# Kernel optimization log

Measured on AMD Instinct MI355X. Metric: run time of the kernel, lower is better.

## Reference

```python
import jax, jax.numpy as jnp
import numpy as np

T, B, S, H, E, V = 100, 64, 602, 1024, 512, 10000


def setup_inputs() -> dict:
    key = jax.random.key(0)
    ks = jax.random.split(key, 12)
    s = 0.02  # small init scale for numerical stability through tanh/sigmoid
    return {
        "tgt": jax.random.randint(ks[0], (T, B, 1), 0, V),
        "memory_bank": jax.random.normal(ks[1], (S, B, H), jnp.float32),
        "h0": jax.random.normal(ks[2], (2, B, H), jnp.float32) * 0.1,
        "c0": jax.random.normal(ks[3], (2, B, H), jnp.float32) * 0.1,
        "embedding": jax.random.normal(ks[4], (V, E), jnp.float32) * s,
        "Wi0": jax.random.normal(ks[5], (4 * H, E + H), jnp.float32) * s,
        "Wh0": jax.random.normal(ks[6], (4 * H, H), jnp.float32) * s,
        "bi0": jnp.zeros((4 * H,), jnp.float32),
        "bh0": jnp.zeros((4 * H,), jnp.float32),
        "Wi1": jax.random.normal(ks[7], (4 * H, H), jnp.float32) * s,
        "Wh1": jax.random.normal(ks[8], (4 * H, H), jnp.float32) * s,
        "bi1": jnp.zeros((4 * H,), jnp.float32),
        "bh1": jnp.zeros((4 * H,), jnp.float32),
        "W_attn": jax.random.normal(ks[9], (H, H), jnp.float32) * s,
        "W_out": jax.random.normal(ks[10], (H, 2 * H), jnp.float32) * s,
    }


def _lstm_cell(x, h, c, Wi, Wh, bi, bh):
    # PyTorch LSTM gate order: i, f, g, o
    g = x @ Wi.T + h @ Wh.T + bi + bh
    i, f, gg, o = jnp.split(g, 4, axis=-1)
    c2 = jax.nn.sigmoid(f) * c + jax.nn.sigmoid(i) * jnp.tanh(gg)
    h2 = jax.nn.sigmoid(o) * jnp.tanh(c2)
    return h2, c2


def reference(tgt, memory_bank, h0, c0, embedding, Wi0, Wh0, bi0, bh0,
              Wi1, Wh1, bi1, bh1, W_attn, W_out):
    emb = embedding[tgt[:, :, 0]]            # [T, B, E]
    M = jnp.transpose(memory_bank, (1, 0, 2))  # [B, S, H]

    def step(carry, e_t):
        hl0, hl1, cl0, cl1, feed = carry
        x = jnp.concatenate([e_t, feed], axis=-1)        # input feeding
        nh0, nc0 = _lstm_cell(x, hl0, cl0, Wi0, Wh0, bi0, bh0)
        nh1, nc1 = _lstm_cell(nh0, hl1, cl1, Wi1, Wh1, bi1, bh1)
        # GlobalAttention 'general': score = (h W) . m
        q = nh1 @ W_attn.T                                # [B, H]
        align = jnp.einsum('bh,bsh->bs', q, M)            # [B, S]
        a = jax.nn.softmax(align, axis=-1)
        ctx = jnp.einsum('bs,bsh->bh', a, M)              # [B, H]
        out = jnp.tanh(jnp.concatenate([ctx, nh1], -1) @ W_out.T)  # attn_h
        return (nh0, nh1, nc0, nc1, out), (out, a)

    init = (h0[0], h0[1], c0[0], c0[1], jnp.zeros((B, H), emb.dtype))
    (_, _, _, _, _), (outs, attns) = jax.lax.scan(step, init, emb)
    return outs, attns  # [T,B,H], [T,B,S]
```

## Files before the change

kernel.cpp:

```cpp
#include <hip/hip_runtime.h>


#define DI __device__ __forceinline__

typedef __attribute__((ext_vector_type(4))) short s4v;
typedef __attribute__((ext_vector_type(8))) short s8v;
typedef __attribute__((ext_vector_type(4))) float f4v;

DI float b2f(short u) {
  unsigned int x = ((unsigned int)(unsigned short)u) << 16;
  float f; __builtin_memcpy(&f, &x, 4); return f;
}
DI short f2b(float f) {
  unsigned int x; __builtin_memcpy(&x, &f, 4);
  return (short)((x + 0x7fffu + ((x >> 16) & 1u)) >> 16);
}
DI s8v cat8(s4v lo, s4v hi) {
  s8v r; r[0]=lo[0];r[1]=lo[1];r[2]=lo[2];r[3]=lo[3];
  r[4]=hi[0];r[5]=hi[1];r[6]=hi[2];r[7]=hi[3]; return r;
}
DI f4v mfma16(s8v a, s8v b, f4v c) {
  return __builtin_amdgcn_mfma_f32_16x16x32_bf16(a, b, c, 0, 0, 0);
}
DI float sigm(float x) { return 1.f / (1.f + __expf(-x)); }

DI unsigned long long ld64c(const void* p) {
  return __hip_atomic_load((const unsigned long long*)p, __ATOMIC_RELAXED,
                           __HIP_MEMORY_SCOPE_SYSTEM);
}
DI void st64c(void* p, unsigned long long v) {
  __hip_atomic_store((unsigned long long*)p, v, __ATOMIC_RELAXED,
                     __HIP_MEMORY_SCOPE_SYSTEM);
}
DI float ldfc(const float* p) {
  return __hip_atomic_load(p, __ATOMIC_RELAXED, __HIP_MEMORY_SCOPE_SYSTEM);
}
DI void stfc(float* p, float v) {
  __hip_atomic_store(p, v, __ATOMIC_RELAXED, __HIP_MEMORY_SCOPE_SYSTEM);
}
DI int ld32c(const int* p) {
  return __hip_atomic_load(p, __ATOMIC_RELAXED, __HIP_MEMORY_SCOPE_SYSTEM);
}
DI void st32c(int* p, int v) {
  __hip_atomic_store(p, v, __ATOMIC_RELAXED, __HIP_MEMORY_SCOPE_SYSTEM);
}
DI void st16c(short* p, short v) {
  asm volatile("global_store_short %0, %1, off sc0 sc1"
               :: "v"(p), "v"((unsigned int)(unsigned short)v) : "memory");
}
DI void st128c(void* p, s8v v) {
  asm volatile("global_store_dwordx4 %0, %1, off sc0 sc1"
               :: "v"(p), "v"(v) : "memory");
}
DI void st128cf(void* p, f4v v) {
  asm volatile("global_store_dwordx4 %0, %1, off sc0 sc1"
               :: "v"(p), "v"(v) : "memory");
}
union U64S { unsigned long long u; short s[4]; };
union U64F { unsigned long long u; float f[2]; };


__global__ void cvt_bf16(const float* __restrict__ src, short* __restrict__ dst, long n8) {
  long i = (long)blockIdx.x * blockDim.x + threadIdx.x;
  long stride = (long)gridDim.x * blockDim.x;
  for (; i < n8; i += stride) {
    const float* s = src + i * 8;
    s8v o;
    #pragma unroll
    for (int j = 0; j < 8; ++j) o[j] = f2b(s[j]);
    *(s8v*)(dst + i * 8) = o;
  }
}

__global__ void pack_w(const float* __restrict__ WA, int Ka,
                       const float* __restrict__ WB, int Kb,
                       short* __restrict__ dst, int N, long total) {
  long i = (long)blockIdx.x * blockDim.x + threadIdx.x;
  long stride = (long)gridDim.x * blockDim.x;
  for (; i < total; i += stride) {
    int c = (int)(i & 3);
    long r = i >> 2;
    int n = (int)(r % N);
    int kt = (int)(r / N);
    int k = kt * 32 + c * 8;
    const float* s = (k < Ka) ? (WA + (size_t)n * Ka + k)
                              : (WB + (size_t)n * Kb + (k - Ka));
    s8v o;
    #pragma unroll
    for (int j = 0; j < 8; ++j) o[j] = f2b(s[j]);
    *(s8v*)(dst + r * 32 + c * 8) = o;
  }
}

__global__ __launch_bounds__(64) void emb_gather(const int* __restrict__ tgt,
                                                 const float* __restrict__ emb,
                                                 short* __restrict__ dst) {
  int tb = blockIdx.x;
  int idx = tgt[tb];
  const float* s = emb + (size_t)idx * 512 + threadIdx.x * 8;
  s8v o;
  #pragma unroll
  for (int j = 0; j < 8; ++j) o[j] = f2b(s[j]);
  *(s8v*)(dst + (size_t)tb * 512 + threadIdx.x * 8) = o;
}

__global__ void init_state(const float* __restrict__ h0, const float* __restrict__ c0,
                           short* __restrict__ h0r, short* __restrict__ h1r,
                           float* __restrict__ c0buf, float* __restrict__ c1buf,
                           short* __restrict__ feedr) {
  int i = blockIdx.x * 256 + threadIdx.x;
  if (i < 65536) {
    h0r[i] = f2b(h0[i]);
    h1r[i] = f2b(h0[65536 + i]);
    int row = i >> 10, col = i & 1023;
    size_t coff = (size_t)((row >> 4) * 64 + (col >> 4)) * 256
                + (row & 15) * 16 + (col & 15);
    c0buf[coff] = c0[i];
    c1buf[coff] = c0[65536 + i];
    feedr[i] = 0;
  }
}


template <int NG>
DI void kloop_il(const short* __restrict__ A, int ld, int nkt,
                 const short* __restrict__ Wp, size_t wkt,
                 f4v* accA, f4v* accB, int rA, int g) {
  if (nkt <= 0) return;
  const short* ap = A + (size_t)rA * ld + 4 * g;
  int kt = 0;
  for (; kt + 1 < nkt; kt += 2) {
    const short* a0 = ap + kt * 32;
    const short* a1 = ap + (kt + 1) * 32;
    const short* b0 = Wp + (size_t)kt * wkt;
    const short* b1 = Wp + (size_t)(kt + 1) * wkt;
    s4v a0lo = *(const s4v*)a0, a0hi = *(const s4v*)(a0 + 16);
    s4v a1lo = *(const s4v*)a1, a1hi = *(const s4v*)(a1 + 16);
    s4v b0lo[NG], b0hi[NG], b1lo[NG], b1hi[NG];
    #pragma unroll
    for (int u = 0; u < NG; ++u) {
      b0lo[u] = *(const s4v*)(b0 + (size_t)u * 32768);
      b0hi[u] = *(const s4v*)(b0 + (size_t)u * 32768 + 16);
      b1lo[u] = *(const s4v*)(b1 + (size_t)u * 32768);
      b1hi[u] = *(const s4v*)(b1 + (size_t)u * 32768 + 16);
    }
    s8v aa = cat8(a0lo, a0hi), ab = cat8(a1lo, a1hi);
    #pragma unroll
    for (int u = 0; u < NG; ++u) {
      accA[u] = mfma16(aa, cat8(b0lo[u], b0hi[u]), accA[u]);
      accB[u] = mfma16(ab, cat8(b1lo[u], b1hi[u]), accB[u]);
    }
  }
  if (kt < nkt) {
    const short* a0 = ap + kt * 32;
    const short* b0 = Wp + (size_t)kt * wkt;
    s8v aa = cat8(*(const s4v*)a0, *(const s4v*)(a0 + 16));
    #pragma unroll
    for (int u = 0; u < NG; ++u)
      accA[u] = mfma16(aa, cat8(*(const s4v*)(b0 + (size_t)u * 32768),
                                *(const s4v*)(b0 + (size_t)u * 32768 + 16)),
                       accA[u]);
  }
}

template <int NG>
DI void seg_gemm(const short* __restrict__ A0, int ld0, int n0,
                 const short* __restrict__ A1, int ld1, int n1,
                 const short* __restrict__ A2, int ld2, int n2,
                 const short* __restrict__ wbase, size_t wkt,
                 int k0, int k1, f4v* accA, f4v* accB, int rA, int g) {
  int s = 0;
  {
    int a = k0 > s ? k0 : s, b = k1 < (s + n0) ? k1 : (s + n0);
    if (a < b) kloop_il<NG>(A0 + (size_t)(a - s) * 32, ld0, b - a,
                            wbase + (size_t)a * wkt, wkt, accA, accB, rA, g);
    s += n0;
  }
  {
    int a = k0 > s ? k0 : s, b = k1 < (s + n1) ? k1 : (s + n1);
    if (a < b) kloop_il<NG>(A1 + (size_t)(a - s) * 32, ld1, b - a,
                            wbase + (size_t)a * wkt, wkt, accA, accB, rA, g);
    s += n1;
  }
  if (n2 > 0) {
    int a = k0 > s ? k0 : s, b = k1 < (s + n2) ? k1 : (s + n2);
    if (a < b) kloop_il<NG>(A2 + (size_t)(a - s) * 32, ld2, b - a,
                            wbase + (size_t)a * wkt, wkt, accA, accB, rA, g);
  }
}

template <int NG>
DI void wave_reduce(f4v* acc, float* smem, int w, int l) {
  #pragma unroll
  for (int t4 = 0; t4 < NG; ++t4)
    *(f4v*)&smem[(w * 64 + l) * 20 + t4 * 4] = acc[t4];
  __syncthreads();
  if (w == 0) {
    #pragma unroll
    for (int t4 = 0; t4 < NG; ++t4) {
      f4v s0 = *(f4v*)&smem[l * 20 + t4 * 4];
      #pragma unroll
      for (int ww = 1; ww < 4; ++ww) {
        f4v v = *(f4v*)&smem[(ww * 64 + l) * 20 + t4 * 4];
        #pragma unroll
        for (int j = 0; j < 4; ++j) s0[j] += v[j];
      }
      acc[t4] = s0;
    }
  }
}


DI void post(int* slot, int val) {
  if (threadIdx.x == 0) st32c(slot, val);
}
DI void wait64(const int* slots, int want) {
  for (;;) {
    int ok = 1;
    if (threadIdx.x < 64) ok = (ld32c(slots + threadIdx.x * 16) >= want);
    if (__syncthreads_and(ok)) break;
    __builtin_amdgcn_s_sleep(4);
  }
}
DI void wait4(const int* slots, int want) {
  for (;;) {
    int ok = 1;
    if (threadIdx.x < 4) ok = (ld32c(slots + threadIdx.x * 16) >= want);
    if (__syncthreads_and(ok)) break;
    __builtin_amdgcn_s_sleep(2);
  }
}


__global__ __launch_bounds__(256, 1) void decoder_k(
    const short* __restrict__ W0p, const short* __restrict__ W1p,
    const short* __restrict__ Wop, const short* __restrict__ Wap,
    const short* __restrict__ emba,
    const float* __restrict__ bi0, const float* __restrict__ bh0,
    const float* __restrict__ bi1, const float* __restrict__ bh1,
    short* h0r, short* h1r, short* feedr, short* ctxr, short* qb,
    float* c0b, float* c1b, float* alg, float* part, float* csum,
    const short* __restrict__ Mb, const float* __restrict__ memf,
    float* out, int useMb, int* bar) {
  __shared__ float smem[5248];
  __shared__ __align__(16) short htile[256];
  __shared__ __align__(16) float ftile[256];
  const int bid = blockIdx.x, tid = threadIdx.x;
  const int w = tid >> 6, l = tid & 63, r15 = l & 15, g = l >> 4;
  const int cs = bid & 63, rt = bid >> 6;
  const int b = bid & 63, chunk = bid >> 6;
  int* s_p1 = bar;
  int* s_p2 = bar + 4096;
  int* s_p3 = bar + 8192;
  int* s_p6 = bar + 12288;
  int* s_p4 = bar + 16384;
  int* s_mg = bar + 20480;
  f4v z = {0.f, 0.f, 0.f, 0.f};

  for (int t = 0; t < 100; ++t) {
    const size_t scur = (size_t)t * 65536, snxt = (size_t)(t + 1) * 65536;

    {
      wait64(s_p6 + rt * 1024, t);
      f4v accA[4] = {z, z, z, z}, accB[4] = {z, z, z, z};
      const short* wbase = W0p + (size_t)(cs * 16 + r15) * 32 + 4 * g;
      seg_gemm<4>(emba + (size_t)t * 64 * 512, 512, 16,
                  feedr + scur, 1024, 32, h0r + scur, 1024, 32,
                  wbase, (size_t)4096 * 32, w * 20, w * 20 + 20,
                  accA, accB, rt * 16 + r15, g);
      #pragma unroll
      for (int u = 0; u < 4; ++u)
        #pragma unroll
        for (int j = 0; j < 4; ++j) accA[u][j] += accB[u][j];
      wave_reduce<4>(accA, smem, w, l);
      if (w == 0) {
        int h = cs * 16 + r15;
        float bs0 = bi0[h] + bh0[h];
        float bs1 = bi0[1024 + h] + bh0[1024 + h];
        float bs2 = bi0[2048 + h] + bh0[2048 + h];
        float bs3 = bi0[3072 + h] + bh0[3072 + h];
        #pragma unroll
        for (int q = 0; q < 4; ++q) {
          size_t coff = (size_t)bid * 256 + (g * 4 + q) * 16 + r15;
          float iv = accA[0][q] + bs0, fv = accA[1][q] + bs1;
          float gv = accA[2][q] + bs2, ov = accA[3][q] + bs3;
          float cn = sigm(fv) * c0b[coff] + sigm(iv) * tanhf(gv);
          float hn = sigm(ov) * tanhf(cn);
          c0b[coff] = cn;
          htile[(g * 4 + q) * 16 + r15] = f2b(hn);
        }
      }
      __syncthreads();
      if (tid < 32) {
        int row = tid >> 1, c8 = (tid & 1) * 8;
        st128c(h0r + snxt + (size_t)(rt * 16 + row) * 1024 + cs * 16 + c8,
               *(const s8v*)&htile[row * 16 + c8]);
      }
      __syncthreads();
      post(s_p1 + (rt * 64 + cs) * 16, t + 1);
    }

    {
      wait64(s_p1 + rt * 1024, t + 1);
      f4v accA[4] = {z, z, z, z}, accB[4] = {z, z, z, z};
      const short* wbase = W1p + (size_t)(cs * 16 + r15) * 32 + 4 * g;
      seg_gemm<4>(h0r + snxt, 1024, 32, h1r + scur, 1024, 32,
                  (const short*)nullptr, 0, 0,
                  wbase, (size_t)4096 * 32, w * 16, w * 16 + 16,
                  accA, accB, rt * 16 + r15, g);
      #pragma unroll
      for (int u = 0; u < 4; ++u)
        #pragma unroll
        for (int j = 0; j < 4; ++j) accA[u][j] += accB[u][j];
      wave_reduce<4>(accA, smem, w, l);
      if (w == 0) {
        int h = cs * 16 + r15;
        float bs0 = bi1[h] + bh1[h];
        float bs1 = bi1[1024 + h] + bh1[1024 + h];
        float bs2 = bi1[2048 + h] + bh1[2048 + h];
        float bs3 = bi1[3072 + h] + bh1[3072 + h];
        #pragma unroll
        for (int q = 0; q < 4; ++q) {
          size_t coff = (size_t)bid * 256 + (g * 4 + q) * 16 + r15;
          float iv = accA[0][q] + bs0, fv = accA[1][q] + bs1;
          float gv = accA[2][q] + bs2, ov = accA[3][q] + bs3;
          float cn = sigm(fv) * c1b[coff] + sigm(iv) * tanhf(gv);
          float hn = sigm(ov) * tanhf(cn);
          c1b[coff] = cn;
          htile[(g * 4 + q) * 16 + r15] = f2b(hn);
        }
      }
      __syncthreads();
      if (tid < 32) {
        int row = tid >> 1, c8 = (tid & 1) * 8;
        st128c(h1r + snxt + (size_t)(rt * 16 + row) * 1024 + cs * 16 + c8,
               *(const s8v*)&htile[row * 16 + c8]);
      }
      __syncthreads();
      post(s_p2 + (rt * 64 + cs) * 16, t + 1);
    }

    {
      wait64(s_p2 + rt * 1024, t + 1);
      f4v accA[1] = {z}, accB[1] = {z};
      const short* wbase = Wap + (size_t)(cs * 16 + r15) * 32 + 4 * g;
      seg_gemm<1>(h1r + snxt, 1024, 32, (const short*)nullptr, 0, 0,
                  (const short*)nullptr, 0, 0,
                  wbase, (size_t)1024 * 32, w * 8, w * 8 + 8,
                  accA, accB, rt * 16 + r15, g);
      #pragma unroll
      for (int j = 0; j < 4; ++j) accA[0][j] += accB[0][j];
      wave_reduce<1>(accA, smem, w, l);
      if (w == 0) {
        #pragma unroll
        for (int q = 0; q < 4; ++q)
          htile[(g * 4 + q) * 16 + r15] = f2b(accA[0][q]);
      }
      __syncthreads();
      if (tid < 32) {
        int row = tid >> 1, c8 = (tid & 1) * 8;
        st128c(qb + (size_t)(rt * 16 + row) * 1024 + cs * 16 + c8,
               *(const s8v*)&htile[row * 16 + c8]);
      }
      __syncthreads();
      post(s_p3 + (rt * 64 + cs) * 16, t + 1);
    }

    {
      wait64(s_p3 + (b >> 4) * 1024, t + 1);
      wait4(s_mg + b * 64, t);
      int s0 = chunk * 151;
      int send = 602 < s0 + 151 ? 602 : s0 + 151;
      const short* qp = qb + (size_t)b * 1024 + l * 16;
      float qf[16];
      #pragma unroll
      for (int c4 = 0; c4 < 4; ++c4) {
        U64S x; x.u = ld64c(qp + c4 * 4);
        #pragma unroll
        for (int j = 0; j < 4; ++j) qf[c4 * 4 + j] = b2f(x.s[j]);
      }
      float o[16];
      #pragma unroll
      for (int j = 0; j < 16; ++j) o[j] = 0.f;
      float ls8 = 0.f;
      for (int s = s0 + w; s < send; s += 16) {
        int sr[4] = {s, s + 4, s + 8, s + 12};
        bool has[4];
        #pragma unroll
        for (int r = 0; r < 4; ++r) has[r] = sr[r] < send;
        float mv[4][16];
        if (useMb) {
          #pragma unroll
          for (int r = 0; r < 4; ++r) {
            int sx = has[r] ? sr[r] : s;
            const short* mp = Mb + ((size_t)sx * 64 + b) * 1024 + l * 16;
            s8v a0 = *(const s8v*)mp, a1 = *(const s8v*)(mp + 8);
            #pragma unroll
            for (int j = 0; j < 8; ++j) {
              mv[r][j] = b2f(a0[j]); mv[r][8 + j] = b2f(a1[j]);
            }
          }
        } else {
          #pragma unroll
          for (int r = 0; r < 4; ++r) {
            int sx = has[r] ? sr[r] : s;
            const float* mp = memf + ((size_t)sx * 64 + b) * 1024 + l * 16;
            f4v a0 = *(const f4v*)mp, a1 = *(const f4v*)(mp + 4);
            f4v a2 = *(const f4v*)(mp + 8), a3 = *(const f4v*)(mp + 12);
            #pragma unroll
            for (int j = 0; j < 4; ++j) {
              mv[r][j] = a0[j]; mv[r][4 + j] = a1[j];
              mv[r][8 + j] = a2[j]; mv[r][12 + j] = a3[j];
            }
          }
        }
        float d[4] = {0.f, 0.f, 0.f, 0.f};
        #pragma unroll
        for (int j = 0; j < 16; ++j) {
          #pragma unroll
          for (int r = 0; r < 4; ++r) d[r] += qf[j] * mv[r][j];
        }
        #pragma unroll
        for (int off = 32; off; off >>= 1) {
          #pragma unroll
          for (int r = 0; r < 4; ++r) d[r] += __shfl_down(d[r], off);
        }
        float p[4];
        #pragma unroll
        for (int r = 0; r < 4; ++r) {
          d[r] = __shfl(d[r], 0);
          p[r] = has[r] ? __expf(fminf(d[r], 80.f) - 8.f) : 0.f;
          ls8 += p[r];
        }
        if (l == 0) {
          #pragma unroll
          for (int r = 0; r < 4; ++r)
            if (has[r]) stfc(alg + b * 602 + sr[r], p[r]);
        }
        #pragma unroll
        for (int j = 0; j < 16; ++j)
          o[j] += p[0] * mv[0][j] + p[1] * mv[1][j]
                + p[2] * mv[2][j] + p[3] * mv[3][j];
      }
      float* pp = part + (size_t)(b * 16 + chunk * 4 + w) * 1024;
      #pragma unroll
      for (int j4 = 0; j4 < 8; ++j4) {
        U64F x; x.f[0] = o[j4 * 2]; x.f[1] = o[j4 * 2 + 1];
        st64c(pp + l * 16 + j4 * 2, x.u);
      }
      if (l == 0) smem[5120 + w] = ls8;
      __syncthreads();
      if (tid == 0)
        stfc(csum + b * 4 + chunk,
             smem[5120] + smem[5121] + smem[5122] + smem[5123]);
      __syncthreads();
      post(s_p4 + (b * 4 + chunk) * 16, t + 1);
      wait4(s_p4 + b * 64, t + 1);
      {
        const float* cs4 = csum + b * 4;
        float L8 = ldfc(cs4) + ldfc(cs4 + 1) + ldfc(cs4 + 2) + ldfc(cs4 + 3);
        float invL = 1.f / L8;
        if (tid < 128) {
          int h = chunk * 256 + tid * 2;
          float a0 = 0.f, a1 = 0.f;
          #pragma unroll
          for (int p = 0; p < 16; ++p) {
            U64F x; x.u = ld64c(part + (size_t)(b * 16 + p) * 1024 + h);
            a0 += x.f[0]; a1 += x.f[1];
          }
          short* cp = ctxr + snxt + (size_t)b * 1024 + h;
          st16c(cp, f2b(a0 * invL));
          st16c(cp + 1, f2b(a1 * invL));
        }
        float* attns = out + 6553600 + (size_t)t * 64 * 602;
        for (int i = s0 + tid; i < send; i += 256)
          stfc(attns + b * 602 + i, ldfc(alg + b * 602 + i) * invL);
      }
      __syncthreads();
      post(s_mg + (b * 4 + chunk) * 16, t + 1);
    }

    {
      wait64(s_mg + rt * 1024, t + 1);
      f4v accA[1] = {z}, accB[1] = {z};
      const short* wbase = Wop + (size_t)(cs * 16 + r15) * 32 + 4 * g;
      seg_gemm<1>(ctxr + snxt, 1024, 32, h1r + snxt, 1024, 32,
                  (const short*)nullptr, 0, 0,
                  wbase, (size_t)1024 * 32, w * 16, w * 16 + 16,
                  accA, accB, rt * 16 + r15, g);
      #pragma unroll
      for (int j = 0; j < 4; ++j) accA[0][j] += accB[0][j];
      wave_reduce<1>(accA, smem, w, l);
      if (w == 0) {
        #pragma unroll
        for (int q = 0; q < 4; ++q) {
          float v = tanhf(accA[0][q]);
          ftile[(g * 4 + q) * 16 + r15] = v;
          htile[(g * 4 + q) * 16 + r15] = f2b(v);
        }
      }
      __syncthreads();
      if (tid < 32) {
        int row = tid >> 1, c8 = (tid & 1) * 8;
        st128c(feedr + snxt + (size_t)(rt * 16 + row) * 1024 + cs * 16 + c8,
               *(const s8v*)&htile[row * 16 + c8]);
      }
      if (tid >= 64 && tid < 128) {
        int x = tid - 64;
        int row = x >> 2, c4 = (x & 3) * 4;
        st128cf(out + (size_t)t * 65536 +
                (size_t)(rt * 16 + row) * 1024 + cs * 16 + c4,
                *(const f4v*)&ftile[row * 16 + c4]);
      }
      __syncthreads();
      post(s_p6 + (rt * 64 + cs) * 16, t + 1);
    }
  }
}


extern "C" void kernel_launch(void* const* d_in, const int* in_sizes, int n_in,
                              void* d_out, int out_size, void* d_ws, size_t ws_size,
                              hipStream_t stream) {
  const int*   tgt  = (const int*)  d_in[0];
  const float* mem  = (const float*)d_in[1];
  const float* h0   = (const float*)d_in[2];
  const float* c0   = (const float*)d_in[3];
  const float* embw = (const float*)d_in[4];
  const float* Wi0  = (const float*)d_in[5];
  const float* Wh0  = (const float*)d_in[6];
  const float* bi0  = (const float*)d_in[7];
  const float* bh0  = (const float*)d_in[8];
  const float* Wi1  = (const float*)d_in[9];
  const float* Wh1  = (const float*)d_in[10];
  const float* bi1  = (const float*)d_in[11];
  const float* bh1  = (const float*)d_in[12];
  const float* Wat  = (const float*)d_in[13];
  const float* Wou  = (const float*)d_in[14];
  float* out = (float*)d_out;

  char* base = (char*)d_ws;
  size_t off = 0;
  auto alloc = [&](size_t bytes) -> void* {
    void* p = base + off;
    off += (bytes + 255) & ~(size_t)255;
    return p;
  };
  const size_t RING = (size_t)101 * 65536;
  int* bar = (int*)alloc(131072);
  short* qb   = (short*)alloc(65536 * 2);
  float* csum = (float*)alloc(64 * 4 * 4);
  float* c0b  = (float*)alloc(65536 * 4);
  float* c1b  = (float*)alloc(65536 * 4);
  float* alg  = (float*)alloc((size_t)64 * 602 * 4);
  float* part = (float*)alloc((size_t)64 * 16 * 1024 * 4);
  short* emba = (short*)alloc((size_t)100 * 64 * 512 * 2);
  short* Wap  = (short*)alloc((size_t)32 * 1024 * 32 * 2);
  short* Wop  = (short*)alloc((size_t)64 * 1024 * 32 * 2);
  short* W1p  = (short*)alloc((size_t)64 * 4096 * 32 * 2);
  short* W0p  = (short*)alloc((size_t)80 * 4096 * 32 * 2);
  short* h0r  = (short*)alloc(RING * 2);
  short* h1r  = (short*)alloc(RING * 2);
  short* feedr= (short*)alloc(RING * 2);
  short* ctxr = (short*)alloc(RING * 2);
  const size_t MBE = (size_t)602 * 64 * 1024;
  bool useMb = (off + MBE * 2 + 256) <= ws_size;
  short* Mb = useMb ? (short*)alloc(MBE * 2) : nullptr;

  hipMemsetAsync(bar, 0, 131072, stream);
  hipLaunchKernelGGL(emb_gather, dim3(6400), dim3(64), 0, stream, tgt, embw, emba);
  hipLaunchKernelGGL(pack_w, dim3(2048), dim3(256), 0, stream, Wi0, 1536, Wh0, 1024,
                     W0p, 4096, (long)80 * 4096 * 4);
  hipLaunchKernelGGL(pack_w, dim3(2048), dim3(256), 0, stream, Wi1, 1024, Wh1, 1024,
                     W1p, 4096, (long)64 * 4096 * 4);
  hipLaunchKernelGGL(pack_w, dim3(1024), dim3(256), 0, stream, Wou, 2048, Wou, 2048,
                     Wop, 1024, (long)64 * 1024 * 4);
  hipLaunchKernelGGL(pack_w, dim3(512), dim3(256), 0, stream, Wat, 1024, Wat, 1024,
                     Wap, 1024, (long)32 * 1024 * 4);
  hipLaunchKernelGGL(init_state, dim3(256), dim3(256), 0, stream, h0, c0,
                     h0r, h1r, c0b, c1b, feedr);
  if (useMb)
    hipLaunchKernelGGL(cvt_bf16, dim3(2048), dim3(256), 0, stream, mem, Mb,
                       (long)(MBE / 8));

  hipLaunchKernelGGL(decoder_k, dim3(256), dim3(256), 0, stream,
                     W0p, W1p, Wop, Wap, emba,
                     bi0, bh0, bi1, bh1,
                     h0r, h1r, feedr, ctxr, qb,
                     c0b, c1b, alg, part, csum,
                     Mb, mem, out, (int)useMb,
                     bar);
}
```

Measured before the change: 7.306 ms.

## Double decoder block to 512 threads, splitting LSTM gates across wave halves

The persistent decoder kernel now launches 512 threads per block (8 waves). The LSTM GEMMs split the four gates into two pairs across wave groups, with each group keeping a four-way K split, and the partial sums are combined through a new shared gate tile. The attention and output projections split K eight ways. The attention scan still uses only the first four waves. The aim is more memory-level parallelism per CU on the latency-bound recurrent GEMMs, at the cost of extra syncthreads, more shared memory, and idle waves during attention.

```diff
diff --git a/kernel.cpp b/kernel.cpp
--- a/kernel.cpp
+++ b/kernel.cpp
@@ -190,17 +190,17 @@
 }
 
 template <int NG>
-DI void wave_reduce(f4v* acc, float* smem, int w, int l) {
+DI void wave_reduce8(f4v* acc, float* smem, int w8, int l) {
   #pragma unroll
   for (int t4 = 0; t4 < NG; ++t4)
-    *(f4v*)&smem[(w * 64 + l) * 20 + t4 * 4] = acc[t4];
+    *(f4v*)&smem[(w8 * 64 + l) * 20 + t4 * 4] = acc[t4];
   __syncthreads();
-  if (w == 0) {
+  if (w8 == 0) {
     #pragma unroll
     for (int t4 = 0; t4 < NG; ++t4) {
       f4v s0 = *(f4v*)&smem[l * 20 + t4 * 4];
       #pragma unroll
-      for (int ww = 1; ww < 4; ++ww) {
+      for (int ww = 1; ww < 8; ++ww) {
         f4v v = *(f4v*)&smem[(ww * 64 + l) * 20 + t4 * 4];
         #pragma unroll
         for (int j = 0; j < 4; ++j) s0[j] += v[j];
@@ -232,7 +232,7 @@
 }
 
 
-__global__ __launch_bounds__(256, 1) void decoder_k(
+__global__ __launch_bounds__(512, 1) void decoder_k(
     const short* __restrict__ W0p, const short* __restrict__ W1p,
     const short* __restrict__ Wop, const short* __restrict__ Wap,
     const short* __restrict__ emba,
@@ -242,11 +242,13 @@
     float* c0b, float* c1b, float* alg, float* part, float* csum,
     const short* __restrict__ Mb, const float* __restrict__ memf,
     float* out, int useMb, int* bar) {
-  __shared__ float smem[5248];
+  __shared__ float smem[10248];
+  __shared__ float gtile[1024];
   __shared__ __align__(16) short htile[256];
   __shared__ __align__(16) float ftile[256];
   const int bid = blockIdx.x, tid = threadIdx.x;
-  const int w = tid >> 6, l = tid & 63, r15 = l & 15, g = l >> 4;
+  const int w8 = tid >> 6, l = tid & 63, r15 = l & 15, g = l >> 4;
+  const int kw = w8 & 3, gh = w8 >> 2;
   const int cs = bid & 63, rt = bid >> 6;
   const int b = bid & 63, chunk = bid >> 6;
   int* s_p1 = bar;
@@ -262,18 +264,38 @@
 
     {
       wait64(s_p6 + rt * 1024, t);
-      f4v accA[4] = {z, z, z, z}, accB[4] = {z, z, z, z};
-      const short* wbase = W0p + (size_t)(cs * 16 + r15) * 32 + 4 * g;
-      seg_gemm<4>(emba + (size_t)t * 64 * 512, 512, 16,
+      f4v accA[2] = {z, z}, accB[2] = {z, z};
+      const short* wbase = W0p + (size_t)(cs * 16 + r15) * 32 + 4 * g
+                         + (size_t)gh * 65536;
+      seg_gemm<2>(emba + (size_t)t * 64 * 512, 512, 16,
                   feedr + scur, 1024, 32, h0r + scur, 1024, 32,
-                  wbase, (size_t)4096 * 32, w * 20, w * 20 + 20,
+                  wbase, (size_t)4096 * 32, kw * 20, kw * 20 + 20,
                   accA, accB, rt * 16 + r15, g);
       #pragma unroll
-      for (int u = 0; u < 4; ++u)
+      for (int u = 0; u < 2; ++u)
         #pragma unroll
         for (int j = 0; j < 4; ++j) accA[u][j] += accB[u][j];
-      wave_reduce<4>(accA, smem, w, l);
-      if (w == 0) {
+      #pragma unroll
+      for (int u = 0; u < 2; ++u)
+        *(f4v*)&smem[(w8 * 64 + l) * 20 + u * 4] = accA[u];
+      __syncthreads();
+      if (kw == 0) {
+        #pragma unroll
+        for (int u = 0; u < 2; ++u) {
+          f4v s0 = *(f4v*)&smem[((gh * 4) * 64 + l) * 20 + u * 4];
+          #pragma unroll
+          for (int kk = 1; kk < 4; ++kk) {
+            f4v v = *(f4v*)&smem[((gh * 4 + kk) * 64 + l) * 20 + u * 4];
+            #pragma unroll
+            for (int j = 0; j < 4; ++j) s0[j] += v[j];
+          }
+          #pragma unroll
+          for (int q = 0; q < 4; ++q)
+            gtile[(2 * gh + u) * 256 + (g * 4 + q) * 16 + r15] = s0[q];
+        }
+      }
+      __syncthreads();
+      if (w8 == 0) {
         int h = cs * 16 + r15;
         float bs0 = bi0[h] + bh0[h];
         float bs1 = bi0[1024 + h] + bh0[1024 + h];
@@ -281,13 +303,16 @@
         float bs3 = bi0[3072 + h] + bh0[3072 + h];
         #pragma unroll
         for (int q = 0; q < 4; ++q) {
-          size_t coff = (size_t)bid * 256 + (g * 4 + q) * 16 + r15;
-          float iv = accA[0][q] + bs0, fv = accA[1][q] + bs1;
-          float gv = accA[2][q] + bs2, ov = accA[3][q] + bs3;
+          int row = g * 4 + q;
+          size_t coff = (size_t)bid * 256 + row * 16 + r15;
+          float iv = gtile[row * 16 + r15] + bs0;
+          float fv = gtile[256 + row * 16 + r15] + bs1;
+          float gv = gtile[512 + row * 16 + r15] + bs2;
+          float ov = gtile[768 + row * 16 + r15] + bs3;
           float cn = sigm(fv) * c0b[coff] + sigm(iv) * tanhf(gv);
           float hn = sigm(ov) * tanhf(cn);
           c0b[coff] = cn;
-          htile[(g * 4 + q) * 16 + r15] = f2b(hn);
+          htile[row * 16 + r15] = f2b(hn);
         }
       }
       __syncthreads();
@@ -302,18 +327,38 @@
 
     {
       wait64(s_p1 + rt * 1024, t + 1);
-      f4v accA[4] = {z, z, z, z}, accB[4] = {z, z, z, z};
-      const short* wbase = W1p + (size_t)(cs * 16 + r15) * 32 + 4 * g;
-      seg_gemm<4>(h0r + snxt, 1024, 32, h1r + scur, 1024, 32,
+      f4v accA[2] = {z, z}, accB[2] = {z, z};
+      const short* wbase = W1p + (size_t)(cs * 16 + r15) * 32 + 4 * g
+                         + (size_t)gh * 65536;
+      seg_gemm<2>(h0r + snxt, 1024, 32, h1r + scur, 1024, 32,
                   (const short*)nullptr, 0, 0,
-                  wbase, (size_t)4096 * 32, w * 16, w * 16 + 16,
+                  wbase, (size_t)4096 * 32, kw * 16, kw * 16 + 16,
                   accA, accB, rt * 16 + r15, g);
       #pragma unroll
-      for (int u = 0; u < 4; ++u)
+      for (int u = 0; u < 2; ++u)
         #pragma unroll
         for (int j = 0; j < 4; ++j) accA[u][j] += accB[u][j];
-      wave_reduce<4>(accA, smem, w, l);
-      if (w == 0) {
+      #pragma unroll
+      for (int u = 0; u < 2; ++u)
+        *(f4v*)&smem[(w8 * 64 + l) * 20 + u * 4] = accA[u];
+      __syncthreads();
+      if (kw == 0) {
+        #pragma unroll
+        for (int u = 0; u < 2; ++u) {
+          f4v s0 = *(f4v*)&smem[((gh * 4) * 64 + l) * 20 + u * 4];
+          #pragma unroll
+          for (int kk = 1; kk < 4; ++kk) {
+            f4v v = *(f4v*)&smem[((gh * 4 + kk) * 64 + l) * 20 + u * 4];
+            #pragma unroll
+            for (int j = 0; j < 4; ++j) s0[j] += v[j];
+          }
+          #pragma unroll
+          for (int q = 0; q < 4; ++q)
+            gtile[(2 * gh + u) * 256 + (g * 4 + q) * 16 + r15] = s0[q];
+        }
+      }
+      __syncthreads();
+      if (w8 == 0) {
         int h = cs * 16 + r15;
         float bs0 = bi1[h] + bh1[h];
         float bs1 = bi1[1024 + h] + bh1[1024 + h];
@@ -321,13 +366,16 @@
         float bs3 = bi1[3072 + h] + bh1[3072 + h];
         #pragma unroll
         for (int q = 0; q < 4; ++q) {
-          size_t coff = (size_t)bid * 256 + (g * 4 + q) * 16 + r15;
-          float iv = accA[0][q] + bs0, fv = accA[1][q] + bs1;
-          float gv = accA[2][q] + bs2, ov = accA[3][q] + bs3;
+          int row = g * 4 + q;
+          size_t coff = (size_t)bid * 256 + row * 16 + r15;
+          float iv = gtile[row * 16 + r15] + bs0;
+          float fv = gtile[256 + row * 16 + r15] + bs1;
+          float gv = gtile[512 + row * 16 + r15] + bs2;
+          float ov = gtile[768 + row * 16 + r15] + bs3;
           float cn = sigm(fv) * c1b[coff] + sigm(iv) * tanhf(gv);
           float hn = sigm(ov) * tanhf(cn);
           c1b[coff] = cn;
-          htile[(g * 4 + q) * 16 + r15] = f2b(hn);
+          htile[row * 16 + r15] = f2b(hn);
         }
       }
       __syncthreads();
@@ -346,12 +394,12 @@
       const short* wbase = Wap + (size_t)(cs * 16 + r15) * 32 + 4 * g;
       seg_gemm<1>(h1r + snxt, 1024, 32, (const short*)nullptr, 0, 0,
                   (const short*)nullptr, 0, 0,
-                  wbase, (size_t)1024 * 32, w * 8, w * 8 + 8,
+                  wbase, (size_t)1024 * 32, w8 * 4, w8 * 4 + 4,
                   accA, accB, rt * 16 + r15, g);
       #pragma unroll
       for (int j = 0; j < 4; ++j) accA[0][j] += accB[0][j];
-      wave_reduce<1>(accA, smem, w, l);
-      if (w == 0) {
+      wave_reduce8<1>(accA, smem, w8, l);
+      if (w8 == 0) {
         #pragma unroll
         for (int q = 0; q < 4; ++q)
           htile[(g * 4 + q) * 16 + r15] = f2b(accA[0][q]);
@@ -371,88 +419,90 @@
       wait4(s_mg + b * 64, t);
       int s0 = chunk * 151;
       int send = 602 < s0 + 151 ? 602 : s0 + 151;
-      const short* qp = qb + (size_t)b * 1024 + l * 16;
-      float qf[16];
-      #pragma unroll
-      for (int c4 = 0; c4 < 4; ++c4) {
-        U64S x; x.u = ld64c(qp + c4 * 4);
-        #pragma unroll
-        for (int j = 0; j < 4; ++j) qf[c4 * 4 + j] = b2f(x.s[j]);
-      }
-      float o[16];
-      #pragma unroll
-      for (int j = 0; j < 16; ++j) o[j] = 0.f;
-      float ls8 = 0.f;
-      for (int s = s0 + w; s < send; s += 16) {
-        int sr[4] = {s, s + 4, s + 8, s + 12};
-        bool has[4];
-        #pragma unroll
-        for (int r = 0; r < 4; ++r) has[r] = sr[r] < send;
-        float mv[4][16];
-        if (useMb) {
+      if (w8 < 4) {
+        const short* qp = qb + (size_t)b * 1024 + l * 16;
+        float qf[16];
+        #pragma unroll
+        for (int c4 = 0; c4 < 4; ++c4) {
+          U64S x; x.u = ld64c(qp + c4 * 4);
+          #pragma unroll
+          for (int j = 0; j < 4; ++j) qf[c4 * 4 + j] = b2f(x.s[j]);
+        }
+        float o[16];
+        #pragma unroll
+        for (int j = 0; j < 16; ++j) o[j] = 0.f;
+        float ls8 = 0.f;
+        for (int s = s0 + w8; s < send; s += 16) {
+          int sr[4] = {s, s + 4, s + 8, s + 12};
+          bool has[4];
+          #pragma unroll
+          for (int r = 0; r < 4; ++r) has[r] = sr[r] < send;
+          float mv[4][16];
+          if (useMb) {
+            #pragma unroll
+            for (int r = 0; r < 4; ++r) {
+              int sx = has[r] ? sr[r] : s;
+              const short* mp = Mb + ((size_t)sx * 64 + b) * 1024 + l * 16;
+              s8v a0 = *(const s8v*)mp, a1 = *(const s8v*)(mp + 8);
+              #pragma unroll
+              for (int j = 0; j < 8; ++j) {
+                mv[r][j] = b2f(a0[j]); mv[r][8 + j] = b2f(a1[j]);
+              }
+            }
+          } else {
+            #pragma unroll
+            for (int r = 0; r < 4; ++r) {
+              int sx = has[r] ? sr[r] : s;
+              const float* mp = memf + ((size_t)sx * 64 + b) * 1024 + l * 16;
+              f4v a0 = *(const f4v*)mp, a1 = *(const f4v*)(mp + 4);
+              f4v a2 = *(const f4v*)(mp + 8), a3 = *(const f4v*)(mp + 12);
+              #pragma unroll
+              for (int j = 0; j < 4; ++j) {
+                mv[r][j] = a0[j]; mv[r][4 + j] = a1[j];
+                mv[r][8 + j] = a2[j]; mv[r][12 + j] = a3[j];
+              }
+            }
+          }
+          float d[4] = {0.f, 0.f, 0.f, 0.f};
+          #pragma unroll
+          for (int j = 0; j < 16; ++j) {
+            #pragma unroll
+            for (int r = 0; r < 4; ++r) d[r] += qf[j] * mv[r][j];
+          }
+          #pragma unroll
+          for (int off = 32; off; off >>= 1) {
+            #pragma unroll
+            for (int r = 0; r < 4; ++r) d[r] += __shfl_down(d[r], off);
+          }
+          float p[4];
           #pragma unroll
           for (int r = 0; r < 4; ++r) {
-            int sx = has[r] ? sr[r] : s;
-            const short* mp = Mb + ((size_t)sx * 64 + b) * 1024 + l * 16;
-            s8v a0 = *(const s8v*)mp, a1 = *(const s8v*)(mp + 8);
+            d[r] = __shfl(d[r], 0);
+            p[r] = has[r] ? __expf(fminf(d[r], 80.f) - 8.f) : 0.f;
+            ls8 += p[r];
+          }
+          if (l == 0) {
             #pragma unroll
-            for (int j = 0; j < 8; ++j) {
-              mv[r][j] = b2f(a0[j]); mv[r][8 + j] = b2f(a1[j]);
-            }
-          }
-        } else {
-          #pragma unroll
-          for (int r = 0; r < 4; ++r) {
-            int sx = has[r] ? sr[r] : s;
-            const float* mp = memf + ((size_t)sx * 64 + b) * 1024 + l * 16;
-            f4v a0 = *(const f4v*)mp, a1 = *(const f4v*)(mp + 4);
-            f4v a2 = *(const f4v*)(mp + 8), a3 = *(const f4v*)(mp + 12);
-            #pragma unroll
-            for (int j = 0; j < 4; ++j) {
-              mv[r][j] = a0[j]; mv[r][4 + j] = a1[j];
-              mv[r][8 + j] = a2[j]; mv[r][12 + j] = a3[j];
-            }
-          }
-        }
-        float d[4] = {0.f, 0.f, 0.f, 0.f};
-        #pragma unroll
-        for (int j = 0; j < 16; ++j) {
-          #pragma unroll
-          for (int r = 0; r < 4; ++r) d[r] += qf[j] * mv[r][j];
-        }
-        #pragma unroll
-        for (int off = 32; off; off >>= 1) {
-          #pragma unroll
-          for (int r = 0; r < 4; ++r) d[r] += __shfl_down(d[r], off);
-        }
-        float p[4];
-        #pragma unroll
-        for (int r = 0; r < 4; ++r) {
-          d[r] = __shfl(d[r], 0);
-          p[r] = has[r] ? __expf(fminf(d[r], 80.f) - 8.f) : 0.f;
-          ls8 += p[r];
-        }
-        if (l == 0) {
-          #pragma unroll
-          for (int r = 0; r < 4; ++r)
-            if (has[r]) stfc(alg + b * 602 + sr[r], p[r]);
-        }
-        #pragma unroll
-        for (int j = 0; j < 16; ++j)
-          o[j] += p[0] * mv[0][j] + p[1] * mv[1][j]
-                + p[2] * mv[2][j] + p[3] * mv[3][j];
-      }
-      float* pp = part + (size_t)(b * 16 + chunk * 4 + w) * 1024;
-      #pragma unroll
-      for (int j4 = 0; j4 < 8; ++j4) {
-        U64F x; x.f[0] = o[j4 * 2]; x.f[1] = o[j4 * 2 + 1];
-        st64c(pp + l * 16 + j4 * 2, x.u);
-      }
-      if (l == 0) smem[5120 + w] = ls8;
+            for (int r = 0; r < 4; ++r)
+              if (has[r]) stfc(alg + b * 602 + sr[r], p[r]);
+          }
+          #pragma unroll
+          for (int j = 0; j < 16; ++j)
+            o[j] += p[0] * mv[0][j] + p[1] * mv[1][j]
+                  + p[2] * mv[2][j] + p[3] * mv[3][j];
+        }
+        float* pp = part + (size_t)(b * 16 + chunk * 4 + w8) * 1024;
+        #pragma unroll
+        for (int j4 = 0; j4 < 8; ++j4) {
+          U64F x; x.f[0] = o[j4 * 2]; x.f[1] = o[j4 * 2 + 1];
+          st64c(pp + l * 16 + j4 * 2, x.u);
+        }
+        if (l == 0) smem[10240 + w8] = ls8;
+      }
       __syncthreads();
       if (tid == 0)
         stfc(csum + b * 4 + chunk,
-             smem[5120] + smem[5121] + smem[5122] + smem[5123]);
+             smem[10240] + smem[10241] + smem[10242] + smem[10243]);
       __syncthreads();
       post(s_p4 + (b * 4 + chunk) * 16, t + 1);
       wait4(s_p4 + b * 64, t + 1);
@@ -473,7 +523,7 @@
           st16c(cp + 1, f2b(a1 * invL));
         }
         float* attns = out + 6553600 + (size_t)t * 64 * 602;
-        for (int i = s0 + tid; i < send; i += 256)
+        for (int i = s0 + tid; i < send; i += 512)
           stfc(attns + b * 602 + i, ldfc(alg + b * 602 + i) * invL);
       }
       __syncthreads();
@@ -486,12 +536,12 @@
       const short* wbase = Wop + (size_t)(cs * 16 + r15) * 32 + 4 * g;
       seg_gemm<1>(ctxr + snxt, 1024, 32, h1r + snxt, 1024, 32,
                   (const short*)nullptr, 0, 0,
-                  wbase, (size_t)1024 * 32, w * 16, w * 16 + 16,
+                  wbase, (size_t)1024 * 32, w8 * 8, w8 * 8 + 8,
                   accA, accB, rt * 16 + r15, g);
       #pragma unroll
       for (int j = 0; j < 4; ++j) accA[0][j] += accB[0][j];
-      wave_reduce<1>(accA, smem, w, l);
-      if (w == 0) {
+      wave_reduce8<1>(accA, smem, w8, l);
+      if (w8 == 0) {
         #pragma unroll
         for (int q = 0; q < 4; ++q) {
           float v = tanhf(accA[0][q]);
@@ -583,7 +633,7 @@
     hipLaunchKernelGGL(cvt_bf16, dim3(2048), dim3(256), 0, stream, mem, Mb,
                        (long)(MBE / 8));
 
-  hipLaunchKernelGGL(decoder_k, dim3(256), dim3(256), 0, stream,
+  hipLaunchKernelGGL(decoder_k, dim3(256), dim3(512), 0, stream,
                      W0p, W1p, Wop, Wap, emba,
                      bi0, bh0, bi1, bh1,
                      h0r, h1r, feedr, ctxr, qb,
```

Measured after the change: 9.944 ms. 36.1% more time.
